# Optimization experiments

Measured on AMD Instinct MI355X. Metric: run time of the kernel, lower is better.

## Reference

```python
import jax, jax.numpy as jnp
import numpy as np

D = 1024
LN_EPS = 1e-5


def setup_inputs() -> dict:
    key = jax.random.key(0)
    k1, k2 = jax.random.split(key)
    L, B = 2048, 8
    x = jax.random.normal(k1, (L, B, D), dtype=jnp.float32)
    c = jnp.zeros((B, D), dtype=jnp.float32)
    W = jax.random.normal(k2, (3 * D, D), dtype=jnp.float32) * (1.0 / np.sqrt(D))
    # bias: forget-gate slice [D:2D] initialized to 1.5, rest zero (matches _init_bias)
    b = jnp.zeros((3 * D,), dtype=jnp.float32).at[D:2 * D].set(1.5)
    ln_g = jnp.ones((D,), dtype=jnp.float32)
    ln_b = jnp.zeros((D,), dtype=jnp.float32)
    return {"x": x, "c": c, "W": W, "b": b, "ln_g": ln_g, "ln_b": ln_b}


def _layernorm(x, g, b):
    mu = jnp.mean(x, axis=-1, keepdims=True)
    var = jnp.mean(jnp.square(x - mu), axis=-1, keepdims=True)
    return (x - mu) * jax.lax.rsqrt(var + LN_EPS) * g + b


def _sru_forward(x, c, W, b, ln_g, ln_b):
    residual = x
    x_norm = _layernorm(x, ln_g, ln_b)          # [L, B, D]
    ufr = jnp.einsum('lbd,ed->lbe', x_norm, W) + b  # [L, B, 3D]
    u, f, r = jnp.split(ufr, 3, axis=-1)
    f_gate = jax.nn.sigmoid(f)
    r_gate = jax.nn.sigmoid(r)
    u_tanh = jnp.tanh(u)

    def step(c_prev, inputs):
        f_t, u_t = inputs
        c_t = f_t * c_prev + (1.0 - f_t) * u_t
        return c_t, c_t

    last_c, c_stack = jax.lax.scan(step, c, (f_gate, u_tanh))  # [L, B, D]
    hs = r_gate * jnp.tanh(c_stack) + (1.0 - r_gate) * x_norm
    return residual + hs, last_c


def reference(x, c, W, b, ln_g, ln_b):
    return _sru_forward(x, c, W, b, ln_g, ln_b)
```

## Files before the change

### kernel.cpp

```cpp
#include <hip/hip_runtime.h>

#define L_DIM 2048
#define B_DIM 8
#define DD    1024
#define M_DIM 16384
#define N_DIM 3072
#define K_DIM 1024
#define CH    8192
#define CH8   1024
#define NSEG  128
#define LSEG  16
#define LN_EPS 1e-5f

typedef __attribute__((ext_vector_type(8))) short bf16x8;
typedef __attribute__((ext_vector_type(8))) unsigned short u16x8;
typedef __attribute__((ext_vector_type(4))) float f32x4;

__device__ __forceinline__ unsigned short f2bf(float f){
  unsigned u = __float_as_uint(f);
  u += 0x7fffu + ((u >> 16) & 1u);
  return (unsigned short)(u >> 16);
}
__device__ __forceinline__ float bf2f(unsigned short h){
  return __uint_as_float(((unsigned)h) << 16);
}
__device__ __forceinline__ float fsigmoid(float z){ return 1.0f/(1.0f + __expf(-z)); }
__device__ __forceinline__ float ftanh(float z){ return 1.0f - 2.0f/(1.0f + __expf(2.0f*z)); }

__global__ __launch_bounds__(256) void ln_kernel(const float* __restrict__ x,
                                                 const float* __restrict__ g,
                                                 const float* __restrict__ bta,
                                                 unsigned short* __restrict__ xn)
{
  int tid  = threadIdx.x;
  int wave = tid >> 6, lane = tid & 63;
  int row  = blockIdx.x * 4 + wave;
  const float4* xr = (const float4*)(x + (size_t)row * DD);
  float4 v[4];
  #pragma unroll
  for (int k = 0; k < 4; k++) v[k] = xr[lane + k * 64];
  float s = 0.f, sq = 0.f;
  #pragma unroll
  for (int k = 0; k < 4; k++) {
    s  += v[k].x + v[k].y + v[k].z + v[k].w;
    sq += v[k].x*v[k].x + v[k].y*v[k].y + v[k].z*v[k].z + v[k].w*v[k].w;
  }
  #pragma unroll
  for (int off = 32; off > 0; off >>= 1) {
    s  += __shfl_down(s,  off, 64);
    sq += __shfl_down(sq, off, 64);
  }
  s  = __shfl(s,  0, 64);
  sq = __shfl(sq, 0, 64);
  float mean = s * (1.0f / DD);
  float var  = sq * (1.0f / DD) - mean * mean;
  float rstd = rsqrtf(var + LN_EPS);
  ushort4* xo = (ushort4*)(xn + (size_t)row * DD);
  #pragma unroll
  for (int k = 0; k < 4; k++) {
    float4 gg = ((const float4*)g)[lane + k * 64];
    float4 bb = ((const float4*)bta)[lane + k * 64];
    ushort4 o;
    o.x = f2bf((v[k].x - mean) * rstd * gg.x + bb.x);
    o.y = f2bf((v[k].y - mean) * rstd * gg.y + bb.y);
    o.z = f2bf((v[k].z - mean) * rstd * gg.z + bb.z);
    o.w = f2bf((v[k].w - mean) * rstd * gg.w + bb.w);
    xo[lane + k * 64] = o;
  }
}

__global__ __launch_bounds__(256) void wconv_kernel(const float* __restrict__ W,
                                                    unsigned short* __restrict__ wb)
{
  int gid = blockIdx.x * 256 + threadIdx.x;
  float4 v = ((const float4*)W)[gid];
  ushort4 o;
  o.x = f2bf(v.x); o.y = f2bf(v.y); o.z = f2bf(v.z); o.w = f2bf(v.w);
  ((ushort4*)wb)[gid] = o;
}

#define BM 256
#define BN 128
#define BK 64
#define LDP 136

#define GLDS16(gp, lp) __builtin_amdgcn_global_load_lds( \
    (const __attribute__((address_space(1))) void*)(gp), \
    (__attribute__((address_space(3))) void*)(lp), 16, 0, 0)

__global__ __launch_bounds__(512, 4) void gemm_gates(const unsigned short* __restrict__ A,
                                                     const unsigned short* __restrict__ Bw,
                                                     const float* __restrict__ bias,
                                                     unsigned short* __restrict__ u_t,
                                                     unsigned short* __restrict__ f_g,
                                                     unsigned short* __restrict__ r_g)
{
  __shared__ unsigned short smem[24576];
  unsigned short* sA = smem;
  unsigned short* sB = smem + BM * BK;
  int tid  = threadIdx.x;
  int wave = tid >> 6, lane = tid & 63;

  int bm0 = blockIdx.x * BM;
  int bn0 = blockIdx.y * BN;

  f32x4 zero = {0.f, 0.f, 0.f, 0.f};
  f32x4 acc[8][2];
  #pragma unroll
  for (int i = 0; i < 8; i++)
    #pragma unroll
    for (int j = 0; j < 2; j++) acc[i][j] = zero;

  int q8  = lane >> 3;
  int rr8 = lane & 7;
  int sch = rr8 ^ q8;
  const unsigned short* a_lane = A  + (size_t)(bm0 + wave * 32 + q8) * K_DIM + sch * 8;
  const unsigned short* b_lane = Bw + (size_t)(bn0 + wave * 16 + q8) * K_DIM + sch * 8;

  int wm = (wave >> 2) * 128, wn = (wave & 3) * 32;
  int fm = lane & 15, quad = lane >> 4;
  int f7 = fm & 7;

  for (int k0 = 0; k0 < K_DIM; k0 += BK) {
    #pragma unroll
    for (int i = 0; i < 4; i++)
      GLDS16(a_lane + (size_t)(i * 8) * K_DIM + k0, &sA[(wave * 32 + i * 8) * BK]);
    #pragma unroll
    for (int i = 0; i < 2; i++)
      GLDS16(b_lane + (size_t)(i * 8) * K_DIM + k0, &sB[(wave * 16 + i * 8) * BK]);
    __syncthreads();

    #pragma unroll
    for (int kk = 0; kk < 2; kk++) {
      int slot = (kk * 4 + quad) ^ f7;
      bf16x8 bfr[2];
      #pragma unroll
      for (int ni = 0; ni < 2; ni++)
        bfr[ni] = *(const bf16x8*)&sB[(wn + ni * 16 + fm) * BK + slot * 8];
      #pragma unroll
      for (int mi = 0; mi < 8; mi++) {
        bf16x8 af = *(const bf16x8*)&sA[(wm + mi * 16 + fm) * BK + slot * 8];
        acc[mi][0] = __builtin_amdgcn_mfma_f32_16x16x32_bf16(af, bfr[0], acc[mi][0], 0, 0, 0);
        acc[mi][1] = __builtin_amdgcn_mfma_f32_16x16x32_bf16(af, bfr[1], acc[mi][1], 0, 0, 0);
      }
    }
    __syncthreads();
  }

  int slice = bn0 >> 10;
  int nd0   = bn0 & 1023;
  unsigned short* dst = (slice == 0) ? u_t : ((slice == 1) ? f_g : r_g);

  #pragma unroll
  for (int h = 0; h < 4; ++h) {
    if ((wave >> 2) == (h >> 1)) {
      #pragma unroll
      for (int ni = 0; ni < 2; ni++) {
        int lcol = wn + ni * 16 + fm;
        float bia = bias[bn0 + lcol];
        #pragma unroll
        for (int mq = 0; mq < 4; mq++) {
          int mi = (h & 1) * 4 + mq;
          #pragma unroll
          for (int reg = 0; reg < 4; reg++) {
            int lrow = mq * 16 + quad * 4 + reg;
            float v = acc[mi][ni][reg] + bia;
            float act = (slice == 0) ? ftanh(v) : fsigmoid(v);
            smem[lrow * LDP + lcol] = f2bf(act);
          }
        }
      }
    }
    __syncthreads();
    #pragma unroll
    for (int it = 0; it < 2; ++it) {
      int row = it * 32 + (tid >> 4);
      int cc  = (tid & 15) * 8;
      u16x8 v = *(const u16x8*)&smem[row * LDP + cc];
      *(u16x8*)(dst + (size_t)(bm0 + h * 64 + row) * DD + nd0 + cc) = v;
    }
    __syncthreads();
  }
}

__global__ __launch_bounds__(256) void scan_pass1(const unsigned short* __restrict__ f_g,
                                                  const unsigned short* __restrict__ u_t,
                                                  unsigned short* __restrict__ P,
                                                  unsigned short* __restrict__ E)
{
  int vc8 = blockIdx.x * 256 + threadIdx.x;
  int seg = blockIdx.y;
  const u16x8* f8 = (const u16x8*)f_g;
  const u16x8* u8 = (const u16x8*)u_t;
  size_t g = (size_t)(seg * LSEG) * CH8 + vc8;
  float p[8], e[8];
  #pragma unroll
  for (int k = 0; k < 8; k++) { p[k] = 1.f; e[k] = 0.f; }
  #pragma unroll 4
  for (int i = 0; i < LSEG; i++) {
    u16x8 ff = f8[g];
    u16x8 uu = u8[g];
    #pragma unroll
    for (int k = 0; k < 8; k++) {
      float fv = bf2f(ff[k]);
      e[k] = fv * e[k] + (1.f - fv) * bf2f(uu[k]);
      p[k] *= fv;
    }
    g += CH8;
  }
  u16x8 pv, ev;
  #pragma unroll
  for (int k = 0; k < 8; k++) { pv[k] = f2bf(p[k]); ev[k] = f2bf(e[k]); }
  ((u16x8*)P)[(size_t)seg * CH8 + vc8] = pv;
  ((u16x8*)E)[(size_t)seg * CH8 + vc8] = ev;
}

__global__ __launch_bounds__(128) void scan_pass2(const unsigned short* __restrict__ P,
                                                  const unsigned short* __restrict__ E,
                                                  const float* __restrict__ c0,
                                                  float* __restrict__ Cini,
                                                  float* __restrict__ lastc)
{
  int ch = blockIdx.x * 128 + threadIdx.x;
  float c = c0[ch];
  #pragma unroll 8
  for (int s = 0; s < NSEG; s++) {
    Cini[(size_t)s * CH + ch] = c;
    c = bf2f(P[(size_t)s * CH + ch]) * c + bf2f(E[(size_t)s * CH + ch]);
  }
  lastc[ch] = c;
}

__global__ __launch_bounds__(256) void scan_pass3(const unsigned short* __restrict__ f_g,
                                                  const unsigned short* __restrict__ u_t,
                                                  const unsigned short* __restrict__ r_g,
                                                  const float* __restrict__ x,
                                                  const unsigned short* __restrict__ xn,
                                                  const float* __restrict__ Cini,
                                                  float* __restrict__ out)
{
  int vc8 = blockIdx.x * 256 + threadIdx.x;
  int seg = blockIdx.y;
  const u16x8* f8 = (const u16x8*)f_g;
  const u16x8* u8 = (const u16x8*)u_t;
  const u16x8* r8 = (const u16x8*)r_g;
  const u16x8* n8 = (const u16x8*)xn;
  const float4* x4 = (const float4*)x;
  float4* o4 = (float4*)out;
  float c[8];
  {
    const float4* C4 = (const float4*)Cini;
    size_t ci = (size_t)seg * (CH / 4) + (size_t)vc8 * 2;
    float4 ca = C4[ci], cb = C4[ci + 1];
    c[0]=ca.x; c[1]=ca.y; c[2]=ca.z; c[3]=ca.w;
    c[4]=cb.x; c[5]=cb.y; c[6]=cb.z; c[7]=cb.w;
  }
  size_t g = (size_t)(seg * LSEG) * CH8 + vc8;
  #pragma unroll 2
  for (int i = 0; i < LSEG; i++) {
    u16x8 ff = f8[g];
    u16x8 uu = u8[g];
    u16x8 rr = r8[g];
    u16x8 nn = n8[g];
    size_t xi = g * 2;
    float4 xa = x4[xi], xb = x4[xi + 1];
    float ov[8];
    #pragma unroll
    for (int k = 0; k < 8; k++) {
      float fv = bf2f(ff[k]);
      c[k] = fv * c[k] + (1.f - fv) * bf2f(uu[k]);
      float rv = bf2f(rr[k]);
      ov[k] = rv * ftanh(c[k]) + (1.f - rv) * bf2f(nn[k]);
    }
    o4[xi]     = (float4){xa.x + ov[0], xa.y + ov[1], xa.z + ov[2], xa.w + ov[3]};
    o4[xi + 1] = (float4){xb.x + ov[4], xb.y + ov[5], xb.z + ov[6], xb.w + ov[7]};
    g += CH8;
  }
}

extern "C" void kernel_launch(void* const* d_in, const int* in_sizes, int n_in,
                              void* d_out, int out_size, void* d_ws, size_t ws_size,
                              hipStream_t stream) {
  const float* x    = (const float*)d_in[0];
  const float* c0   = (const float*)d_in[1];
  const float* W    = (const float*)d_in[2];
  const float* bias = (const float*)d_in[3];
  const float* ln_g = (const float*)d_in[4];
  const float* ln_b = (const float*)d_in[5];
  float* out = (float*)d_out;

  char* ws = (char*)d_ws;
  unsigned short* xn  = (unsigned short*)(ws);
  unsigned short* wb  = (unsigned short*)(ws + 33554432ULL);
  unsigned short* u_t = (unsigned short*)(ws + 39845888ULL);
  unsigned short* f_g = (unsigned short*)(ws + 73400320ULL);
  unsigned short* r_g = (unsigned short*)(ws + 106954752ULL);
  unsigned short* Pseg = (unsigned short*)(ws + 33554432ULL);
  unsigned short* Eseg = (unsigned short*)(ws + 35651584ULL);
  float* Cini = (float*)(ws + 140509184ULL);

  ln_kernel   <<<M_DIM / 4, 256, 0, stream>>>(x, ln_g, ln_b, xn);
  wconv_kernel<<<N_DIM, 256, 0, stream>>>(W, wb);
  gemm_gates  <<<dim3(M_DIM / BM, N_DIM / BN), 512, 0, stream>>>(xn, wb, bias, u_t, f_g, r_g);
  scan_pass1  <<<dim3(CH8 / 256, NSEG), 256, 0, stream>>>(f_g, u_t, Pseg, Eseg);
  scan_pass2  <<<CH / 128, 128, 0, stream>>>(Pseg, Eseg, c0, Cini, out + (size_t)M_DIM * DD);
  scan_pass3  <<<dim3(CH8 / 256, NSEG), 256, 0, stream>>>(f_g, u_t, r_g, x, xn, Cini, out);
}
```

Before: 211.4 us.

## Double-buffer A tiles and hand-schedule LDS reads and MFMAs in gates GEMM

Rewrites the gates GEMM main loop as a software pipeline: A tiles are double-buffered in LDS and prefetched two iterations ahead, while the B tile is reloaded each iteration. Fragment reads use inline ds_read_b128 with immediate offsets, explicit waitcnt and scheduling barriers, and setprio around the MFMA bursts. The aim is to hide global-load latency behind MFMA work and cut the two full syncs per k-step. It raises LDS use to 80KB per block, which may limit occupancy below the launch-bounds target, and the hand-placed waits are fragile.

After: 206.5 us. -2.3%, faster.

```diff
diff --git a/kernel.cpp b/kernel.cpp
--- a/kernel.cpp
+++ b/kernel.cpp
@@ -82,11 +82,22 @@
 #define BM 256
 #define BN 128
 #define BK 64
+#define NT 16
 #define LDP 136
 
 #define GLDS16(gp, lp) __builtin_amdgcn_global_load_lds( \
     (const __attribute__((address_space(1))) void*)(gp), \
     (__attribute__((address_space(3))) void*)(lp), 16, 0, 0)
+
+#define SBAR()   __builtin_amdgcn_s_barrier()
+#define SCHED0() __builtin_amdgcn_sched_barrier(0)
+#define WAIT_LGKM0() do { asm volatile("s_waitcnt lgkmcnt(0)" ::: "memory"); SCHED0(); } while(0)
+#define WAIT_VM(N)   do { asm volatile("s_waitcnt vmcnt(" #N ")" ::: "memory"); SCHED0(); } while(0)
+
+#define DSR(dst, addr, IMM) \
+  asm volatile("ds_read_b128 %0, %1 offset:" #IMM : "=v"(dst) : "v"(addr))
+
+#define MFMA(a, b, c) __builtin_amdgcn_mfma_f32_16x16x32_bf16((a), (b), (c), 0, 0, 0)
 
 __global__ __launch_bounds__(512, 4) void gemm_gates(const unsigned short* __restrict__ A,
                                                      const unsigned short* __restrict__ Bw,
@@ -95,14 +106,12 @@
                                                      unsigned short* __restrict__ f_g,
                                                      unsigned short* __restrict__ r_g)
 {
-  __shared__ unsigned short smem[24576];
-  unsigned short* sA = smem;
-  unsigned short* sB = smem + BM * BK;
-  int tid  = threadIdx.x;
-  int wave = tid >> 6, lane = tid & 63;
-
-  int bm0 = blockIdx.x * BM;
-  int bn0 = blockIdx.y * BN;
+  __shared__ unsigned short smem[40960];
+  const int tid  = threadIdx.x;
+  const int wave = tid >> 6, lane = tid & 63;
+
+  const int bm0 = blockIdx.x * BM;
+  const int bn0 = blockIdx.y * BN;
 
   f32x4 zero = {0.f, 0.f, 0.f, 0.f};
   f32x4 acc[8][2];
@@ -111,44 +120,78 @@
     #pragma unroll
     for (int j = 0; j < 2; j++) acc[i][j] = zero;
 
-  int q8  = lane >> 3;
-  int rr8 = lane & 7;
-  int sch = rr8 ^ q8;
+  const int q8  = lane >> 3;
+  const int rr8 = lane & 7;
+  const int sch = rr8 ^ q8;
   const unsigned short* a_lane = A  + (size_t)(bm0 + wave * 32 + q8) * K_DIM + sch * 8;
   const unsigned short* b_lane = Bw + (size_t)(bn0 + wave * 16 + q8) * K_DIM + sch * 8;
 
-  int wm = (wave >> 2) * 128, wn = (wave & 3) * 32;
-  int fm = lane & 15, quad = lane >> 4;
-  int f7 = fm & 7;
-
-  for (int k0 = 0; k0 < K_DIM; k0 += BK) {
-    #pragma unroll
-    for (int i = 0; i < 4; i++)
-      GLDS16(a_lane + (size_t)(i * 8) * K_DIM + k0, &sA[(wave * 32 + i * 8) * BK]);
-    #pragma unroll
-    for (int i = 0; i < 2; i++)
-      GLDS16(b_lane + (size_t)(i * 8) * K_DIM + k0, &sB[(wave * 16 + i * 8) * BK]);
-    __syncthreads();
-
-    #pragma unroll
-    for (int kk = 0; kk < 2; kk++) {
-      int slot = (kk * 4 + quad) ^ f7;
-      bf16x8 bfr[2];
-      #pragma unroll
-      for (int ni = 0; ni < 2; ni++)
-        bfr[ni] = *(const bf16x8*)&sB[(wn + ni * 16 + fm) * BK + slot * 8];
-      #pragma unroll
-      for (int mi = 0; mi < 8; mi++) {
-        bf16x8 af = *(const bf16x8*)&sA[(wm + mi * 16 + fm) * BK + slot * 8];
-        acc[mi][0] = __builtin_amdgcn_mfma_f32_16x16x32_bf16(af, bfr[0], acc[mi][0], 0, 0, 0);
-        acc[mi][1] = __builtin_amdgcn_mfma_f32_16x16x32_bf16(af, bfr[1], acc[mi][1], 0, 0, 0);
-      }
-    }
-    __syncthreads();
-  }
-
-  int slice = bn0 >> 10;
-  int nd0   = bn0 & 1023;
+  const int wm = (wave >> 2) * 128, wn = (wave & 3) * 32;
+  const int fm = lane & 15, quad = lane >> 4;
+  const int f7 = fm & 7;
+
+#define STAGE_A(BUF, T) do { \
+  GLDS16(a_lane + (size_t)(T) * BK,                      &smem[(BUF)*16384 + (wave * 32 +  0) * BK]); \
+  GLDS16(a_lane + (size_t)(T) * BK + (size_t) 8 * K_DIM, &smem[(BUF)*16384 + (wave * 32 +  8) * BK]); \
+  GLDS16(a_lane + (size_t)(T) * BK + (size_t)16 * K_DIM, &smem[(BUF)*16384 + (wave * 32 + 16) * BK]); \
+  GLDS16(a_lane + (size_t)(T) * BK + (size_t)24 * K_DIM, &smem[(BUF)*16384 + (wave * 32 + 24) * BK]); \
+} while(0)
+
+#define STAGE_B(T) do { \
+  GLDS16(b_lane + (size_t)(T) * BK,                      &smem[32768 + (wave * 16 + 0) * BK]); \
+  GLDS16(b_lane + (size_t)(T) * BK + (size_t) 8 * K_DIM, &smem[32768 + (wave * 16 + 8) * BK]); \
+} while(0)
+
+#define COMPUTE_KK(AADDR, BADDR) do { \
+  bf16x8 b0f, b1f, a0f, a1f, a2f, a3f; \
+  DSR(b0f, (BADDR), 0); DSR(b1f, (BADDR), 2048); \
+  DSR(a0f, (AADDR), 0);    DSR(a1f, (AADDR), 2048); \
+  DSR(a2f, (AADDR), 4096); DSR(a3f, (AADDR), 6144); \
+  WAIT_LGKM0(); \
+  acc[0][0] = MFMA(a0f, b0f, acc[0][0]); acc[0][1] = MFMA(a0f, b1f, acc[0][1]); \
+  acc[1][0] = MFMA(a1f, b0f, acc[1][0]); acc[1][1] = MFMA(a1f, b1f, acc[1][1]); \
+  acc[2][0] = MFMA(a2f, b0f, acc[2][0]); acc[2][1] = MFMA(a2f, b1f, acc[2][1]); \
+  acc[3][0] = MFMA(a3f, b0f, acc[3][0]); acc[3][1] = MFMA(a3f, b1f, acc[3][1]); \
+  DSR(a0f, (AADDR), 8192);  DSR(a1f, (AADDR), 10240); \
+  DSR(a2f, (AADDR), 12288); DSR(a3f, (AADDR), 14336); \
+  WAIT_LGKM0(); \
+  acc[4][0] = MFMA(a0f, b0f, acc[4][0]); acc[4][1] = MFMA(a0f, b1f, acc[4][1]); \
+  acc[5][0] = MFMA(a1f, b0f, acc[5][0]); acc[5][1] = MFMA(a1f, b1f, acc[5][1]); \
+  acc[6][0] = MFMA(a2f, b0f, acc[6][0]); acc[6][1] = MFMA(a2f, b1f, acc[6][1]); \
+  acc[7][0] = MFMA(a3f, b0f, acc[7][0]); acc[7][1] = MFMA(a3f, b1f, acc[7][1]); \
+} while(0)
+
+  const unsigned slot0 = (unsigned)((quad ^ f7) << 4);
+  const unsigned aBase = (unsigned)((wm + fm) * 128) + slot0;
+  const unsigned bBase = 65536u + (unsigned)((wn + fm) * 128) + slot0;
+
+  STAGE_B(0);
+  STAGE_A(0, 0);
+  STAGE_A(1, 1);
+  WAIT_VM(4);
+  SBAR();
+
+  #pragma unroll
+  for (int t = 0; t < NT; ++t) {
+    const int cb = t & 1;
+    const unsigned cbB = (unsigned)(cb * 32768);
+    __builtin_amdgcn_s_setprio(1);
+    COMPUTE_KK(cbB + aBase,         bBase);
+    COMPUTE_KK((cbB + aBase) ^ 64u, bBase ^ 64u);
+    __builtin_amdgcn_s_setprio(0);
+    SCHED0();
+    SBAR();
+    if (t + 1 < NT) STAGE_B(t + 1);
+    if (t + 2 < NT) STAGE_A(cb, t + 2);
+    SCHED0();
+    if      (t <  NT - 2) WAIT_VM(4);
+    else if (t == NT - 2) WAIT_VM(0);
+    SBAR();
+  }
+  __syncthreads();
+
+  const int slice = bn0 >> 10;
+  const int nd0   = bn0 & 1023;
   unsigned short* dst = (slice == 0) ? u_t : ((slice == 1) ? f_g : r_g);
 
   #pragma unroll
```
